# Performance work log

Measured on AMD Instinct MI355X. Metric: run time of the kernel, lower is better.

Reference implementation:

```python
import jax, jax.numpy as jnp
import numpy as np

B, L, H, W = 16, 16, 64, 64
NUM_CODES = 64


def setup_inputs() -> dict:
    key = jax.random.key(0)
    k1, k2 = jax.random.split(key)
    z = jax.random.normal(k1, (B, L, H, W), dtype=jnp.float32)
    # nn.Embedding(latent_dim, num_codes).weight -> [latent_dim, num_codes]
    codes_w = jax.random.normal(k2, (L, NUM_CODES), dtype=jnp.float32)
    return {"z": z, "codes_w": codes_w}


def reference(z, codes_w):
    # z: [B, L, H, W] -> h: [B, H, W, L]
    h = jnp.transpose(z, (0, 2, 3, 1))
    # broadcast abs-distance to every code: [B, H, W, L, C]
    distances = jnp.abs(h[..., None] - codes_w)
    # Softmin over code axis == softmax of negated distances
    symbol_probs = jax.nn.softmax(-distances, axis=-1)
    # soft quantization: probability-weighted codebook values -> [B, H, W, L]
    soft_symbols = jnp.sum(symbol_probs * codes_w, axis=-1)
    # hard assignment: nearest code per (position, latent channel)
    idxes = jnp.argmin(distances, axis=-1)  # [B, H, W, L] int
    # gather codebook value per latent row (equivalent of take with row offsets)
    hard_symbols = jnp.take_along_axis(
        codes_w[None, None, None], idxes[..., None], axis=4
    )[..., 0]
    return soft_symbols, hard_symbols, idxes
```

## Files before the change

kernel.cpp:

```cpp
#include <hip/hip_runtime.h>


namespace {
constexpr int kL = 16;
constexpr int kC = 64;
constexpr int kHW = 64 * 64;
constexpr int kN = 16 * kHW * kL;
constexpr int kStride = 68;
constexpr float kLog2e = 1.44269504088896340736f;
}

__global__ __launch_bounds__(256) void soft_to_hard_kernel(
    const float* __restrict__ z,
    const float* __restrict__ codes,
    float* __restrict__ out)
{
    __shared__ float wl[kL * kStride];
    __shared__ float pl[kL * kStride];
    __shared__ float ql[kL * kStride];

    const int tid = threadIdx.x;

    {
        const int base = tid << 2;
        const int l = base >> 6;
        const int c = base & 63;
        const float4 wv = *reinterpret_cast<const float4*>(codes + base);
        const int o = l * kStride + c;
        wl[o + 0] = wv.x; wl[o + 1] = wv.y; wl[o + 2] = wv.z; wl[o + 3] = wv.w;
        pl[o + 0] = exp2f(wv.x * kLog2e);
        pl[o + 1] = exp2f(wv.y * kLog2e);
        pl[o + 2] = exp2f(wv.z * kLog2e);
        pl[o + 3] = exp2f(wv.w * kLog2e);
        ql[o + 0] = exp2f(-wv.x * kLog2e);
        ql[o + 1] = exp2f(-wv.y * kLog2e);
        ql[o + 2] = exp2f(-wv.z * kLog2e);
        ql[o + 3] = exp2f(-wv.w * kLog2e);
    }
    __syncthreads();

    const int gid = blockIdx.x * 256 + tid;
    const int l   = gid & (kL - 1);
    const int bhw = gid >> 4;
    const int b   = gid >> 16;
    const int hw  = bhw & (kHW - 1);

    const float zv = z[(b << 16) + (l << 12) + hw];

    const float t    = zv * kLog2e;
    const float E    = exp2f(t);
    const float Einv = exp2f(-t);

    const float* __restrict__ wr = wl + l * kStride;
    const float* __restrict__ pr = pl + l * kStride;
    const float* __restrict__ qr = ql + l * kStride;

    float mind = 3.4e38f;
    int   idx  = 0;
    float sum  = 0.0f;
    float wsum = 0.0f;

#define STEP(wc, pc, qc, cc)                                  \
    {                                                         \
        const float d = __builtin_fabsf(zv - (wc));           \
        idx  = (d < mind) ? (cc) : idx;                       \
        mind = fminf(d, mind);                                \
        const float e = fminf(E * (qc), Einv * (pc));         \
        sum += e;                                             \
        wsum = __builtin_fmaf(e, (wc), wsum);                 \
    }

#pragma unroll
    for (int c0 = 0; c0 < kC; c0 += 4) {
        const float4 wv = *reinterpret_cast<const float4*>(wr + c0);
        const float4 pv = *reinterpret_cast<const float4*>(pr + c0);
        const float4 qv = *reinterpret_cast<const float4*>(qr + c0);
        STEP(wv.x, pv.x, qv.x, c0 + 0);
        STEP(wv.y, pv.y, qv.y, c0 + 1);
        STEP(wv.z, pv.z, qv.z, c0 + 2);
        STEP(wv.w, pv.w, qv.w, c0 + 3);
    }
#undef STEP

    const float soft = wsum / sum;
    const float hard = wr[idx];

    out[gid]          = soft;
    out[kN + gid]     = hard;
    out[2 * kN + gid] = (float)idx;
}

extern "C" void kernel_launch(void* const* d_in, const int* in_sizes, int n_in,
                              void* d_out, int out_size, void* d_ws, size_t ws_size,
                              hipStream_t stream) {
    const float* z     = (const float*)d_in[0];
    const float* codes = (const float*)d_in[1];
    float* out = (float*)d_out;

    const int threads = 256;
    const int blocks  = kN / threads;
    soft_to_hard_kernel<<<blocks, threads, 0, stream>>>(z, codes, out);
}
```

Before: 72.27 us.

## Replace per-code scan with sorted-codebook binary search and prefix-sum softmin tables

A prep kernel sorts each latent row's codebook and builds prefix/suffix sums of exp(w) and exp(-w) (plain and value-weighted). The main kernel then binary-searches each z in the sorted row. It gets the softmin sums in closed form from the split point and picks the nearest code from the two neighbours. This replaces the 64-step per-element loop with about 7 LDS lookups. Each thread now handles 4 elements and the launch has fewer, larger blocks, at the cost of an extra kernel launch and possible float differences from the prefix-sum reassociation.

```diff
diff --git a/kernel.cpp b/kernel.cpp
--- a/kernel.cpp
+++ b/kernel.cpp
@@ -6,98 +6,147 @@
 constexpr int kC = 64;
 constexpr int kHW = 64 * 64;
 constexpr int kN = 16 * kHW * kL;
-constexpr int kStride = 68;
 constexpr float kLog2e = 1.44269504088896340736f;
+constexpr float kBig = 3.0e38f;
+
+constexpr int kRowEnt = 65;
+constexpr int kCandF4 = kL * kRowEnt;
+constexpr int kTblF4 = 2 * kCandF4;
+constexpr int kWsStride = 67;
+constexpr int kWsF4 = (kL * kWsStride + 3) / 4;
 }
 
-__global__ __launch_bounds__(256) void soft_to_hard_kernel(
+__global__ __launch_bounds__(64) void prep_kernel(
+    const float* __restrict__ codes, float4* __restrict__ wsout)
+{
+    const int l = blockIdx.x;
+    const int lane = threadIdx.x;
+    const float w = codes[l * kC + lane];
+
+    int rank = 0;
+#pragma unroll
+    for (int j = 0; j < kC; ++j) {
+        const float wj = __shfl(w, j);
+        rank += (wj < w || (wj == w && j < lane)) ? 1 : 0;
+    }
+
+    __shared__ float sw[kC];
+    __shared__ int so[kC];
+    sw[rank] = w;
+    so[rank] = lane;
+    __syncthreads();
+    const float wsrt = sw[lane];
+    const int osrt = so[lane];
+
+    const float p = exp2f(wsrt * kLog2e);
+    const float q = exp2f(-wsrt * kLog2e);
+    const float pw = p * wsrt;
+    const float qw = q * wsrt;
+
+    float ip = p, ipw = pw, sq = q, sqw = qw;
+#pragma unroll
+    for (int d = 1; d < 64; d <<= 1) {
+        float t;
+        t = __shfl_up(ip, d);    if (lane >= d) ip += t;
+        t = __shfl_up(ipw, d);   if (lane >= d) ipw += t;
+        t = __shfl_down(sq, d);  if (lane < 64 - d) sq += t;
+        t = __shfl_down(sqw, d); if (lane < 64 - d) sqw += t;
+    }
+    float Pexc = __shfl_up(ip, 1);
+    float PWexc = __shfl_up(ipw, 1);
+    if (lane == 0) { Pexc = 0.0f; PWexc = 0.0f; }
+
+    float4* cand = wsout;
+    float4* pqt = wsout + kCandF4;
+    float* wpk = reinterpret_cast<float*>(wsout + kTblF4);
+
+    pqt[l * kRowEnt + lane] = make_float4(Pexc, sq, PWexc, sqw);
+    float wprev = __shfl_up(wsrt, 1);
+    int oprev = __shfl_up(osrt, 1);
+    if (lane == 0) { wprev = -kBig; oprev = 0; }
+    cand[l * kRowEnt + lane] =
+        make_float4(wprev, wsrt, (float)oprev, (float)osrt);
+    if (lane == 63) {
+        pqt[l * kRowEnt + 64] = make_float4(ip, 0.0f, ipw, 0.0f);
+        cand[l * kRowEnt + 64] = make_float4(wsrt, kBig, (float)osrt, 0.0f);
+    }
+    wpk[l * kWsStride + lane] = wsrt;
+}
+
+__global__ __launch_bounds__(256, 4) void soft_to_hard_kernel(
     const float* __restrict__ z,
-    const float* __restrict__ codes,
+    const float4* __restrict__ tbl_g,
     float* __restrict__ out)
 {
-    __shared__ float wl[kL * kStride];
-    __shared__ float pl[kL * kStride];
-    __shared__ float ql[kL * kStride];
+    __shared__ float4 tbl[kTblF4];
+    __shared__ float4 swr4[kWsF4];
 
     const int tid = threadIdx.x;
+    const int l = tid & (kL - 1);
+    const int base = blockIdx.x * 1024 + tid;
 
-    {
-        const int base = tid << 2;
-        const int l = base >> 6;
-        const int c = base & 63;
-        const float4 wv = *reinterpret_cast<const float4*>(codes + base);
-        const int o = l * kStride + c;
-        wl[o + 0] = wv.x; wl[o + 1] = wv.y; wl[o + 2] = wv.z; wl[o + 3] = wv.w;
-        pl[o + 0] = exp2f(wv.x * kLog2e);
-        pl[o + 1] = exp2f(wv.y * kLog2e);
-        pl[o + 2] = exp2f(wv.z * kLog2e);
-        pl[o + 3] = exp2f(wv.w * kLog2e);
-        ql[o + 0] = exp2f(-wv.x * kLog2e);
-        ql[o + 1] = exp2f(-wv.y * kLog2e);
-        ql[o + 2] = exp2f(-wv.z * kLog2e);
-        ql[o + 3] = exp2f(-wv.w * kLog2e);
+    float zv[4];
+#pragma unroll
+    for (int i = 0; i < 4; ++i) {
+        const int gid = base + 256 * i;
+        const int b = gid >> 16;
+        const int hw = (gid >> 4) & (kHW - 1);
+        zv[i] = z[(b << 16) + (l << 12) + hw];
     }
+
+    for (int t = tid; t < kTblF4; t += 256) tbl[t] = tbl_g[t];
+    for (int t = tid; t < kWsF4; t += 256) swr4[t] = tbl_g[kTblF4 + t];
     __syncthreads();
 
-    const int gid = blockIdx.x * 256 + tid;
-    const int l   = gid & (kL - 1);
-    const int bhw = gid >> 4;
-    const int b   = gid >> 16;
-    const int hw  = bhw & (kHW - 1);
+    const float* wrow = reinterpret_cast<const float*>(swr4) + l * kWsStride;
+    const float4* crow = tbl + l * kRowEnt;
+    const float4* prow = tbl + kCandF4 + l * kRowEnt;
 
-    const float zv = z[(b << 16) + (l << 12) + hw];
-
-    const float t    = zv * kLog2e;
-    const float E    = exp2f(t);
-    const float Einv = exp2f(-t);
-
-    const float* __restrict__ wr = wl + l * kStride;
-    const float* __restrict__ pr = pl + l * kStride;
-    const float* __restrict__ qr = ql + l * kStride;
-
-    float mind = 3.4e38f;
-    int   idx  = 0;
-    float sum  = 0.0f;
-    float wsum = 0.0f;
-
-#define STEP(wc, pc, qc, cc)                                  \
-    {                                                         \
-        const float d = __builtin_fabsf(zv - (wc));           \
-        idx  = (d < mind) ? (cc) : idx;                       \
-        mind = fminf(d, mind);                                \
-        const float e = fminf(E * (qc), Einv * (pc));         \
-        sum += e;                                             \
-        wsum = __builtin_fmaf(e, (wc), wsum);                 \
+    int k[4] = {0, 0, 0, 0};
+#pragma unroll
+    for (int s = 32; s >= 1; s >>= 1) {
+#pragma unroll
+        for (int i = 0; i < 4; ++i)
+            if (wrow[k[i] + s - 1] <= zv[i]) k[i] += s;
     }
+#pragma unroll
+    for (int i = 0; i < 4; ++i)
+        if (wrow[k[i]] <= zv[i]) k[i] += 1;
 
 #pragma unroll
-    for (int c0 = 0; c0 < kC; c0 += 4) {
-        const float4 wv = *reinterpret_cast<const float4*>(wr + c0);
-        const float4 pv = *reinterpret_cast<const float4*>(pr + c0);
-        const float4 qv = *reinterpret_cast<const float4*>(qr + c0);
-        STEP(wv.x, pv.x, qv.x, c0 + 0);
-        STEP(wv.y, pv.y, qv.y, c0 + 1);
-        STEP(wv.z, pv.z, qv.z, c0 + 2);
-        STEP(wv.w, pv.w, qv.w, c0 + 3);
+    for (int i = 0; i < 4; ++i) {
+        const int gid = base + 256 * i;
+        const float zi = zv[i];
+        const float t = zi * kLog2e;
+        const float E = exp2f(t);
+        const float Ei = exp2f(-t);
+
+        const float4 pq = prow[k[i]];
+        const float sum = Ei * pq.x + E * pq.y;
+        const float wsum = Ei * pq.z + E * pq.w;
+        const float soft = wsum / sum;
+
+        const float4 cd = crow[k[i]];
+        const float dl = zi - cd.x;
+        const float dr = cd.y - zi;
+        const bool left = (dl < dr) || ((dl == dr) && (cd.z < cd.w));
+        const float hard = left ? cd.x : cd.y;
+        const float idxf = left ? cd.z : cd.w;
+
+        out[gid] = soft;
+        out[kN + gid] = hard;
+        out[2 * kN + gid] = idxf;
     }
-#undef STEP
-
-    const float soft = wsum / sum;
-    const float hard = wr[idx];
-
-    out[gid]          = soft;
-    out[kN + gid]     = hard;
-    out[2 * kN + gid] = (float)idx;
 }
 
 extern "C" void kernel_launch(void* const* d_in, const int* in_sizes, int n_in,
                               void* d_out, int out_size, void* d_ws, size_t ws_size,
                               hipStream_t stream) {
-    const float* z     = (const float*)d_in[0];
+    const float* z = (const float*)d_in[0];
     const float* codes = (const float*)d_in[1];
     float* out = (float*)d_out;
+    float4* tbl = (float4*)d_ws;
 
-    const int threads = 256;
-    const int blocks  = kN / threads;
-    soft_to_hard_kernel<<<blocks, threads, 0, stream>>>(z, codes, out);
+    prep_kernel<<<16, 64, 0, stream>>>(codes, tbl);
+    soft_to_hard_kernel<<<1024, 256, 0, stream>>>(z, tbl, out);
 }
```

Measured after the change: 69.90 us. 3.3% less time.
